# Optimization experiments

Hardware: AMD Instinct MI355X
Metric: run time of the kernel (lower is better)

## Reference

```python
import jax, jax.numpy as jnp
import numpy as np

D_MODEL = 2048
NQ = 16      # query heads
NKV = 4      # kv heads (GQA)
DH = 128     # content head dim
DR = 64      # rope head dim
DKV = 512    # kv latent dim
DQC = 1536   # q latent dim
B, S = 2, 2048
DT = DH + DR


def rotate_half(x):
    x1, x2 = jnp.split(x, 2, axis=-1)
    return jnp.concatenate([-x2, x1], axis=-1)


def setup_inputs() -> dict:
    key = jax.random.key(0)
    ks = jax.random.split(key, 10)
    sc = 0.02
    x = jax.random.normal(ks[0], (B, S, D_MODEL), jnp.float32)
    positions = jnp.arange(S, dtype=jnp.int32)
    # standard RoPE cache over the rope subspace
    inv_freq = 1.0 / (10000.0 ** (jnp.arange(0, DR, 2, dtype=jnp.float32) / DR))
    ang = positions.astype(jnp.float32)[:, None] * inv_freq[None, :]   # [S, DR/2]
    emb = jnp.concatenate([ang, ang], axis=-1)                         # [S, DR]
    cos_cache = jnp.cos(emb)
    sin_cache = jnp.sin(emb)
    attn_mask = jnp.tril(jnp.ones((S, S), dtype=bool))                 # causal, True=attend
    # weights stored [in, out] (torch Linear weight transposed)
    W_DKV = sc * jax.random.normal(ks[1], (D_MODEL, DKV), jnp.float32)
    W_UK = sc * jax.random.normal(ks[2], (DKV, NKV * DH), jnp.float32)
    W_UV = sc * jax.random.normal(ks[3], (DKV, NKV * DH), jnp.float32)
    W_DQ = sc * jax.random.normal(ks[4], (D_MODEL, DQC), jnp.float32)
    W_UQ = sc * jax.random.normal(ks[5], (DQC, NQ * DH), jnp.float32)
    W_KR = sc * jax.random.normal(ks[6], (D_MODEL, NKV * DR), jnp.float32)
    W_QR = sc * jax.random.normal(ks[7], (D_MODEL, NQ * DR), jnp.float32)
    W_O = sc * jax.random.normal(ks[8], (NQ * DH, D_MODEL), jnp.float32)
    return {"x": x, "cos_cache": cos_cache, "sin_cache": sin_cache,
            "positions": positions, "attn_mask": attn_mask,
            "W_DKV": W_DKV, "W_UK": W_UK, "W_UV": W_UV, "W_DQ": W_DQ,
            "W_UQ": W_UQ, "W_KR": W_KR, "W_QR": W_QR, "W_O": W_O}


def reference(x, cos_cache, sin_cache, positions, attn_mask,
              W_DKV, W_UK, W_UV, W_DQ, W_UQ, W_KR, W_QR, W_O):
    b, s, _ = x.shape
    cos = cos_cache[positions][None, None]  # [1,1,S,DR]
    sin = sin_cache[positions][None, None]
    # low-rank KV latent (this is the MLA cache)
    c_kv = x @ W_DKV                                                 # [B,S,DKV]
    K_rope = (x @ W_KR).reshape(b, s, NKV, DR).transpose(0, 2, 1, 3)  # [B,NKV,S,DR]
    K_rope = K_rope * cos + rotate_half(K_rope) * sin
    # decompress K/V content from latent
    K_content = (c_kv @ W_UK).reshape(b, s, NKV, DH).transpose(0, 2, 1, 3)  # [B,NKV,S,DH]
    V = (c_kv @ W_UV).reshape(b, s, NKV, DH).transpose(0, 2, 1, 3)          # [B,NKV,S,DH]
    # queries via low-rank path + rope subspace
    c_q = x @ W_DQ
    Q_content = (c_q @ W_UQ).reshape(b, s, NQ, DH).transpose(0, 2, 1, 3)    # [B,NQ,S,DH]
    Q_rope = (x @ W_QR).reshape(b, s, NQ, DR).transpose(0, 2, 1, 3)         # [B,NQ,S,DR]
    Q_rope = Q_rope * cos + rotate_half(Q_rope) * sin
    Q = jnp.concatenate([Q_content, Q_rope], axis=-1)   # [B,NQ,S,DT]
    K = jnp.concatenate([K_content, K_rope], axis=-1)   # [B,NKV,S,DT]
    # GQA: group query heads over shared kv heads (no materialized repeat)
    G = NQ // NKV
    Qg = Q.reshape(b, NKV, G, s, DT)
    scores = jnp.einsum('bkgsd,bktd->bkgst', Qg, K) / np.float32(np.sqrt(DT))
    scores = jnp.where(attn_mask[None, None, None], scores, -jnp.inf)
    w = jax.nn.softmax(scores, axis=-1)
    attn = jnp.einsum('bkgst,bktd->bkgsd', w, V)         # [B,NKV,G,S,DH]
    attn = attn.reshape(b, NQ, s, DH).transpose(0, 2, 1, 3).reshape(b, s, NQ * DH)
    out = attn @ W_O                                     # [B,S,D_MODEL]
    return out, c_kv, K_rope
```

## Files before the change

### kernel.cpp

```cpp
#include <hip/hip_runtime.h>
#include <stdint.h>

typedef unsigned short u16;
typedef unsigned int u32;

#define B_    2
#define S_    2048
#define NQ_   16
#define NKV_  4
#define DH_   128
#define DR_   64
#define DT_   192
#define M_    4096

using short8 = __attribute__((ext_vector_type(8))) short;
using f32x4  = __attribute__((ext_vector_type(4))) float;
using half8  = __attribute__((ext_vector_type(8))) _Float16;
using u16x4  = __attribute__((ext_vector_type(4))) u16;

__device__ __forceinline__ float cl(float f) {
    return fminf(fmaxf(f, -3.38e38f), 3.38e38f);
}
__device__ __forceinline__ u16 f2b(float f) {
    union { float f; u32 u; } v; v.f = f;
    u32 u = v.u;
    return (u16)((u + 0x7fffu + ((u >> 16) & 1u)) >> 16);
}
__device__ __forceinline__ void gload16(const void* g, void* l) {
    __builtin_amdgcn_global_load_lds(
        (const __attribute__((address_space(1))) void*)g,
        (__attribute__((address_space(3))) void*)l,
        16, 0, 0);
}

__device__ __forceinline__ void wt_body(const float* __restrict__ W,
                                        _Float16* __restrict__ T,
                                        int K, int N, int kx, int ny,
                                        float (*tile)[33]) {
    int k0 = kx * 32, n0 = ny * 32;
    int tx = threadIdx.x, ty = threadIdx.y;
#pragma unroll
    for (int i = 0; i < 32; i += 8)
        tile[ty + i][tx] = W[(size_t)(k0 + ty + i) * N + n0 + tx];
    __syncthreads();
#pragma unroll
    for (int i = 0; i < 32; i += 8)
        T[(size_t)(n0 + ty + i) * K + k0 + tx] = (_Float16)tile[tx][ty + i];
}

__global__ __launch_bounds__(256) void prep_all(const float* __restrict__ x,
                                                _Float16* __restrict__ xf,
                                                const float* __restrict__ W_DKV,
                                                const float* __restrict__ W_KR,
                                                const float* __restrict__ W_DQ,
                                                const float* __restrict__ W_QR,
                                                const float* __restrict__ W_UQ,
                                                const float* __restrict__ W_UK,
                                                const float* __restrict__ W_UV,
                                                const float* __restrict__ W_O,
                                                _Float16* __restrict__ Wmeg,
                                                _Float16* __restrict__ Wuq,
                                                _Float16* __restrict__ Wukv,
                                                _Float16* __restrict__ Wo) {
    __shared__ float tile[32][33];
    const int id = blockIdx.x;
    if (id < 1024) {
        wt_body(W_DKV, Wmeg, 2048, 512, id & 63, id >> 6, tile);
    } else if (id < 1536) {
        int l = id - 1024;
        wt_body(W_KR, Wmeg + (size_t)512 * 2048, 2048, 256, l & 63, l >> 6, tile);
    } else if (id < 4608) {
        int l = id - 1536;
        wt_body(W_DQ, Wmeg + (size_t)768 * 2048, 2048, 1536, l & 63, l >> 6, tile);
    } else if (id < 6656) {
        int l = id - 4608;
        wt_body(W_QR, Wmeg + (size_t)2304 * 2048, 2048, 1024, l & 63, l >> 6, tile);
    } else if (id < 9728) {
        int l = id - 6656;
        wt_body(W_UQ, Wuq, 1536, 2048, l % 48, l / 48, tile);
    } else if (id < 9984) {
        int l = id - 9728;
        wt_body(W_UK, Wukv, 512, 512, l & 15, l >> 4, tile);
    } else if (id < 10240) {
        int l = id - 9984;
        wt_body(W_UV, Wukv + (size_t)512 * 512, 512, 512, l & 15, l >> 4, tile);
    } else if (id < 14336) {
        int l = id - 10240;
        wt_body(W_O, Wo, 2048, 2048, l & 63, l >> 6, tile);
    } else {
        int l = id - 14336;
        int t1 = threadIdx.y * 32 + threadIdx.x;
        size_t i = ((size_t)l * 256 + t1) * 8;
        float4 a = *(const float4*)(x + i);
        float4 b4 = *(const float4*)(x + i + 4);
        float va[8] = {a.x, a.y, a.z, a.w, b4.x, b4.y, b4.z, b4.w};
        half8 f;
#pragma unroll
        for (int j = 0; j < 8; ++j) f[j] = (_Float16)va[j];
        *(half8*)(xf + i) = f;
    }
}

__device__ __forceinline__ void gemm_body(const _Float16* __restrict__ A, int lda,
                                          const _Float16* __restrict__ Bt,
                                          void* p0, void* p1, void* p2,
                                          void* p3, void* p4,
                                          float cscale, int mode,
                                          int N, int K, int bx,
                                          _Float16* lA, _Float16* lB) {
    const int t = threadIdx.x, lane = t & 63, w = t >> 6;
    const int quad = lane >> 4, l16 = lane & 15;
    const int wr = w >> 1, wc = w & 1;
    const int m0 = blockIdx.y * 128, n0 = bx * 128;
    f32x4 acc[4][4] = {};

    for (int kt = 0; kt < K; kt += 32) {
        __syncthreads();
#pragma unroll
        for (int c = 0; c < 2; ++c) {
            const int chunk = c * 256 + t;
            const int row = chunk >> 2, co = (chunk & 3) * 8;
            const int lofs = (c * 256 + w * 64) * 8;
            gload16(A + (size_t)(m0 + row) * lda + kt + co, lA + lofs);
            gload16(Bt + (size_t)(n0 + row) * K + kt + co, lB + lofs);
        }
        __syncthreads();
        half8 af[4], bf4[4];
#pragma unroll
        for (int i = 0; i < 4; ++i) {
            af[i]  = *(const half8*)&lA[(wr * 64 + i * 16 + l16) * 32 + quad * 8];
            bf4[i] = *(const half8*)&lB[(wc * 64 + i * 16 + l16) * 32 + quad * 8];
        }
#pragma unroll
        for (int i = 0; i < 4; ++i)
#pragma unroll
            for (int j = 0; j < 4; ++j)
                acc[i][j] = __builtin_amdgcn_mfma_f32_16x16x32_f16(af[i], bf4[j], acc[i][j], 0, 0, 0);
    }
#pragma unroll
    for (int i = 0; i < 4; ++i)
#pragma unroll
        for (int j = 0; j < 4; ++j) {
            const int mbase = m0 + wr * 64 + i * 16 + quad * 4;
            const int nn = n0 + wc * 64 + j * 16 + l16;
            if (mode == 0) {
                float* C = (float*)p0;
#pragma unroll
                for (int r = 0; r < 4; ++r)
                    C[(size_t)(mbase + r) * N + nn] = cl(acc[i][j][r]);
            } else if (mode == 2) {
                u16* Q = (u16*)p0;
                const int h = nn >> 7, dcol = nn & 127;
#pragma unroll
                for (int r = 0; r < 4; ++r)
                    Q[(size_t)(mbase + r) * 3072 + h * 192 + dcol] =
                        f2b(acc[i][j][r] * cscale);
            } else if (mode == 3) {
                const int bb = mbase >> 11, s = mbase & 2047;
                if (nn < 512) {
                    u16* Kp = (u16*)p0;
                    const int kv = nn >> 7, d = nn & 127;
                    const size_t rb = ((size_t)((bb * 4 + kv) * 2048 + s)) * 192 + d;
#pragma unroll
                    for (int r = 0; r < 4; ++r)
                        Kp[rb + (size_t)r * 192] = f2b(acc[i][j][r]);
                } else {
                    u16* Vt = (u16*)p1;
                    const int e = nn - 512, kv = e >> 7, d = e & 127;
                    u16x4 pk;
                    pk[0] = f2b(acc[i][j][0]); pk[1] = f2b(acc[i][j][1]);
                    pk[2] = f2b(acc[i][j][2]); pk[3] = f2b(acc[i][j][3]);
                    *(u16x4*)&((u16*)Vt)[((size_t)((bb * 4 + kv) * 128 + d)) * 2048 + s] = pk;
                }
            } else {
                if (nn < 512) {
                    float* ckv = (float*)p0;
                    _Float16* ckf = (_Float16*)p1;
#pragma unroll
                    for (int r = 0; r < 4; ++r) {
                        float v = acc[i][j][r];
                        ckv[(size_t)(mbase + r) * 512 + nn] = cl(v);
                        ckf[(size_t)(mbase + r) * 512 + nn] = (_Float16)v;
                    }
                } else if (nn < 768) {
                    float* krr = (float*)p2;
#pragma unroll
                    for (int r = 0; r < 4; ++r)
                        krr[(size_t)(mbase + r) * 256 + (nn - 512)] = acc[i][j][r];
                } else if (nn < 2304) {
                    _Float16* dqc = (_Float16*)p3;
#pragma unroll
                    for (int r = 0; r < 4; ++r)
                        dqc[(size_t)(mbase + r) * 1536 + (nn - 768)] = (_Float16)acc[i][j][r];
                } else {
                    _Float16* qrf = (_Float16*)p4;
#pragma unroll
                    for (int r = 0; r < 4; ++r)
                        qrf[(size_t)(mbase + r) * 1024 + (nn - 2304)] = (_Float16)acc[i][j][r];
                }
            }
        }
}

__global__ __launch_bounds__(256) void gemm_f16(const _Float16* __restrict__ A, int lda,
                                                const _Float16* __restrict__ Bt,
                                                void* p0, void* p1, void* p2,
                                                void* p3, void* p4,
                                                float cscale, int mode,
                                                int N, int K) {
    __shared__ __align__(16) _Float16 lA[128 * 32];
    __shared__ __align__(16) _Float16 lB[128 * 32];
    gemm_body(A, lda, Bt, p0, p1, p2, p3, p4, cscale, mode, N, K, blockIdx.x, lA, lB);
}

__global__ __launch_bounds__(256) void gemm_uqkv(const _Float16* __restrict__ dqc,
                                                 const _Float16* __restrict__ Wuq,
                                                 u16* __restrict__ qb16, float sc,
                                                 const _Float16* __restrict__ ckf,
                                                 const _Float16* __restrict__ Wukv,
                                                 u16* __restrict__ Kp,
                                                 u16* __restrict__ Vt) {
    __shared__ __align__(16) _Float16 lA[128 * 32];
    __shared__ __align__(16) _Float16 lB[128 * 32];
    const int bx = blockIdx.x;
    if (bx < 16)
        gemm_body(dqc, 1536, Wuq, qb16, nullptr, nullptr, nullptr, nullptr,
                  sc, 2, 2048, 1536, bx, lA, lB);
    else
        gemm_body(ckf, 512, Wukv, Kp, Vt, nullptr, nullptr, nullptr,
                  1.f, 3, 1024, 512, bx - 16, lA, lB);
}

__global__ __launch_bounds__(256) void rope_all(const _Float16* __restrict__ qrf,
                                                const float* __restrict__ krr,
                                                const float* __restrict__ cosc,
                                                const float* __restrict__ sinc,
                                                const int* __restrict__ pos,
                                                u16* __restrict__ qb16,
                                                float* __restrict__ Krope,
                                                u16* __restrict__ Kp) {
    const float sc = 0.07216878364870322f;
    if ((int)blockIdx.x < 8192) {
        int t = blockIdx.x * 256 + threadIdx.x;
        int d = t & 31, h = (t >> 5) & 15, rowi = t >> 9;
        int s = rowi & 2047;
        int p = pos[s];
        float c1 = cosc[p * 64 + d],      s1 = sinc[p * 64 + d];
        float c2 = cosc[p * 64 + 32 + d], s2 = sinc[p * 64 + 32 + d];
        const _Float16* base = qrf + (size_t)rowi * 1024 + h * 64;
        float x1 = (float)base[d];
        float x2 = (float)base[d + 32];
        u16* q = qb16 + (size_t)rowi * 3072 + h * 192 + 128;
        q[d]      = f2b((x1 * c1 - x2 * s1) * sc);
        q[d + 32] = f2b((x2 * c2 + x1 * s2) * sc);
    } else {
        int t = (blockIdx.x - 8192) * 256 + threadIdx.x;
        int d = t & 31, kv = (t >> 5) & 3, rowi = t >> 7;
        int b = rowi >> 11, s = rowi & 2047;
        int p = pos[s];
        float c1 = cosc[p * 64 + d],      s1 = sinc[p * 64 + d];
        float c2 = cosc[p * 64 + 32 + d], s2 = sinc[p * 64 + 32 + d];
        float x1 = krr[(size_t)rowi * 256 + kv * 64 + d];
        float x2 = krr[(size_t)rowi * 256 + kv * 64 + 32 + d];
        float o1 = x1 * c1 - x2 * s1;
        float o2 = x2 * c2 + x1 * s2;
        int g = b * NKV_ + kv;
        size_t ob = ((size_t)(g * S_) + s) * 64;
        Krope[ob + d]      = cl(o1);
        Krope[ob + 32 + d] = cl(o2);
        u16* kp = Kp + ((size_t)(g * S_ + s)) * 192 + 128;
        kp[d]      = f2b(o1);
        kp[32 + d] = f2b(o2);
    }
}

__global__ __launch_bounds__(256) void attn_mfma(const u16* __restrict__ qb16,
                                                 const u16* __restrict__ Kp,
                                                 const u16* __restrict__ Vt,
                                                 _Float16* __restrict__ atf) {
    __shared__ __align__(16) u16 lK[64 * 200];
    __shared__ __align__(16) u16 lVt[144 * 72];
    __shared__ __align__(16) u16 lP[4][16 * 72];

    const int t = threadIdx.x, lane = t & 63, w = t >> 6;
    const int quad = lane >> 4, l16 = lane & 15;
    const int id = blockIdx.x;
    const int g = id & 7;
    const int b = g >> 2;
    const int k = id >> 3;
    const int h = (g & 3) * 4 + (k & 3);
    const int px = k >> 2;

#pragma unroll
    for (int c = 0; c < 4; ++c) {
        int i = c * 256 + t;
        int rr = 128 + (i >> 6), ccol = i & 63;
        lVt[rr * 72 + ccol] = (rr == 128) ? (u16)0x3F80 : (u16)0;
    }

    for (int ph = 0; ph < 2; ++ph) {
        const int qt = ph ? px : (31 - px);
        const int q0 = qt * 64;
        const int iw = q0 + w * 16;

        short8 qf[6];
        {
            const u16* qp = qb16 + ((size_t)(b * S_ + iw + l16)) * 3072 + h * 192;
#pragma unroll
            for (int kc = 0; kc < 6; ++kc)
                qf[kc] = *(const short8*)&qp[kc * 32 + quad * 8];
        }

        f32x4 O9[9] = {};
        float mr[4] = {-1e30f, -1e30f, -1e30f, -1e30f};

        const int ntile = qt + 1;
        for (int tile = 0; tile < ntile; ++tile) {
            const int j0 = tile * 64;
            __syncthreads();
#pragma unroll
            for (int c = 0; c < 6; ++c) {
                int seg = c * 256 + t;
                int row = seg / 24, ch = (seg % 24) * 8;
                *(uint4*)&lK[row * 200 + ch] =
                    *(const uint4*)&Kp[((size_t)g * S_ + j0 + row) * 192 + ch];
            }
#pragma unroll
            for (int c = 0; c < 4; ++c) {
                int seg = c * 256 + t;
                int d = seg >> 3, ch = (seg & 7) * 8;
                *(uint4*)&lVt[d * 72 + ch] =
                    *(const uint4*)&Vt[((size_t)g * 128 + d) * S_ + j0 + ch];
            }
            __syncthreads();

            f32x4 s4[4];
            __builtin_amdgcn_s_setprio(1);
#pragma unroll
            for (int cc = 0; cc < 4; ++cc) {
                f32x4 sx = {};
#pragma unroll
                for (int kc = 0; kc < 6; ++kc) {
                    short8 kf = *(const short8*)&lK[(cc * 16 + l16) * 200 + kc * 32 + quad * 8];
                    sx = __builtin_amdgcn_mfma_f32_16x16x32_bf16(qf[kc], kf, sx, 0, 0, 0);
                }
                s4[cc] = sx;
            }
            __builtin_amdgcn_s_setprio(0);

            float sv[4][4];
#pragma unroll
            for (int cc = 0; cc < 4; ++cc)
#pragma unroll
                for (int r = 0; r < 4; ++r) {
                    int ir = iw + quad * 4 + r;
                    sv[cc][r] = (j0 + cc * 16 + l16 <= ir) ? s4[cc][r] : -1e30f;
                }
            float tm[4];
#pragma unroll
            for (int r = 0; r < 4; ++r)
                tm[r] = fmaxf(fmaxf(sv[0][r], sv[1][r]), fmaxf(sv[2][r], sv[3][r]));
#pragma unroll
            for (int m = 1; m < 16; m <<= 1)
#pragma unroll
                for (int r = 0; r < 4; ++r) tm[r] = fmaxf(tm[r], __shfl_xor(tm[r], m));
            int small = (tm[0] <= mr[0] + 8.f) && (tm[1] <= mr[1] + 8.f) &&
                        (tm[2] <= mr[2] + 8.f) && (tm[3] <= mr[3] + 8.f);
            if (!__all(small)) {
                float al[4];
#pragma unroll
                for (int r = 0; r < 4; ++r) {
                    float mn = fmaxf(mr[r], tm[r]);
                    al[r] = __expf(mr[r] - mn);
                    mr[r] = mn;
                }
#pragma unroll
                for (int dc = 0; dc < 9; ++dc)
#pragma unroll
                    for (int r = 0; r < 4; ++r) O9[dc][r] *= al[r];
            }
            float p[4][4];
#pragma unroll
            for (int cc = 0; cc < 4; ++cc)
#pragma unroll
                for (int r = 0; r < 4; ++r)
                    p[cc][r] = __expf(sv[cc][r] - mr[r]);
#pragma unroll
            for (int cc = 0; cc < 4; ++cc)
#pragma unroll
                for (int r = 0; r < 4; ++r)
                    lP[w][(quad * 4 + r) * 72 + cc * 16 + l16] = f2b(p[cc][r]);
            short8 pf0 = *(const short8*)&lP[w][l16 * 72 + quad * 8];
            short8 pf1 = *(const short8*)&lP[w][l16 * 72 + 32 + quad * 8];
            __builtin_amdgcn_s_setprio(1);
#pragma unroll
            for (int dc = 0; dc < 9; ++dc) {
                short8 vf0 = *(const short8*)&lVt[(dc * 16 + l16) * 72 + quad * 8];
                short8 vf1 = *(const short8*)&lVt[(dc * 16 + l16) * 72 + 32 + quad * 8];
                O9[dc] = __builtin_amdgcn_mfma_f32_16x16x32_bf16(pf0, vf0, O9[dc], 0, 0, 0);
                O9[dc] = __builtin_amdgcn_mfma_f32_16x16x32_bf16(pf1, vf1, O9[dc], 0, 0, 0);
            }
            __builtin_amdgcn_s_setprio(0);
        }
        float inv[4];
#pragma unroll
        for (int r = 0; r < 4; ++r) {
            float lr = __shfl(O9[8][r], quad * 16);
            inv[r] = 1.f / fmaxf(lr, 1e-30f);
        }
#pragma unroll
        for (int dc = 0; dc < 8; ++dc)
#pragma unroll
            for (int r = 0; r < 4; ++r) {
                int ir = iw + quad * 4 + r;
                atf[((size_t)(b * S_ + ir)) * 2048 + h * 128 + dc * 16 + l16] =
                    (_Float16)cl(O9[dc][r] * inv[r]);
            }
    }
}

extern "C" void kernel_launch(void* const* d_in, const int* in_sizes, int n_in,
                              void* d_out, int out_size, void* d_ws, size_t ws_size,
                              hipStream_t stream) {
    const float* x     = (const float*)d_in[0];
    const float* cosc  = (const float*)d_in[1];
    const float* sinc  = (const float*)d_in[2];
    const int*   pos   = (const int*)d_in[3];
    const float* W_DKV = (const float*)d_in[5];
    const float* W_UK  = (const float*)d_in[6];
    const float* W_UV  = (const float*)d_in[7];
    const float* W_DQ  = (const float*)d_in[8];
    const float* W_UQ  = (const float*)d_in[9];
    const float* W_KR  = (const float*)d_in[10];
    const float* W_QR  = (const float*)d_in[11];
    const float* W_O   = (const float*)d_in[12];
    (void)ws_size;

    float* outp      = (float*)d_out;
    float* ckv_out   = outp + 8388608;
    float* krope_out = outp + 10485760;

    char* w = (char*)d_ws;
    auto alloc = [&](size_t bytes) { char* p = w; w += bytes; return p; };
    _Float16* xf   = (_Float16*)alloc(16777216);
    _Float16* ckf  = (_Float16*)alloc(4194304);
    float*    krr  = (float*)alloc(4194304);
    _Float16* dqc  = (_Float16*)alloc(12582912);
    _Float16* qrf  = (_Float16*)alloc(8388608);
    u16*      qb16 = (u16*)alloc(25165824);
    u16*      Kp   = (u16*)alloc(6291456);
    u16*      Vt   = (u16*)alloc(4194304);
    _Float16* atf  = (_Float16*)alloc(16777216);
    _Float16* Wmeg = (_Float16*)alloc(13631488);
    _Float16* Wuq  = (_Float16*)alloc(6291456);
    _Float16* Wukv = (_Float16*)alloc(1048576);
    _Float16* Wo   = (_Float16*)alloc(8388608);

    const float sc = 0.07216878364870322f;

    prep_all<<<18432, dim3(32, 8), 0, stream>>>(x, xf,
                                                W_DKV, W_KR, W_DQ, W_QR,
                                                W_UQ, W_UK, W_UV, W_O,
                                                Wmeg, Wuq, Wukv, Wo);

    gemm_f16<<<dim3(26, 32), 256, 0, stream>>>(xf, 2048, Wmeg,
                                               ckv_out, ckf, krr, dqc, qrf,
                                               1.f, 6, 3328, 2048);
    gemm_uqkv<<<dim3(24, 32), 256, 0, stream>>>(dqc, Wuq, qb16, sc,
                                                ckf, Wukv, Kp, Vt);

    rope_all<<<10240, 256, 0, stream>>>(qrf, krr, cosc, sinc, pos,
                                        qb16, krope_out, Kp);

    attn_mfma<<<512, 256, 0, stream>>>(qb16, Kp, Vt, atf);
    gemm_f16<<<dim3(16, 32), 256, 0, stream>>>(atf, 2048, Wo,
                                               outp, nullptr, nullptr, nullptr, nullptr,
                                               1.f, 0, 2048, 2048);
}
```

Baseline: 484.1 us.

## Add 256x256 swizzled-LDS GEMM kernel for large projections

Adds a new 512-thread GEMM kernel with 256x256 output tiles, a K-step of 64, XOR-swizzled LDS layout and a grouped block-index remap for L2 locality. It is used for the fused down-projection, the Q up-projection and the output projection. The small KV up-projection stays on the old 128x128 kernel, which now runs as a separate launch instead of being merged with the Q up-projection. Larger tiles raise data reuse per block and cut LDS bank conflicts, but they launch fewer blocks (128–208), which may leave many of the 256 CUs idle, and they raise register and LDS pressure.

Result: no change. 482.5 us (-0.3%).

```diff
diff --git a/kernel.cpp b/kernel.cpp
--- a/kernel.cpp
+++ b/kernel.cpp
@@ -103,8 +103,7 @@
 
 __device__ __forceinline__ void gemm_body(const _Float16* __restrict__ A, int lda,
                                           const _Float16* __restrict__ Bt,
-                                          void* p0, void* p1, void* p2,
-                                          void* p3, void* p4,
+                                          void* p0, void* p1,
                                           float cscale, int mode,
                                           int N, int K, int bx,
                                           _Float16* lA, _Float16* lB) {
@@ -143,19 +142,7 @@
         for (int j = 0; j < 4; ++j) {
             const int mbase = m0 + wr * 64 + i * 16 + quad * 4;
             const int nn = n0 + wc * 64 + j * 16 + l16;
-            if (mode == 0) {
-                float* C = (float*)p0;
-#pragma unroll
-                for (int r = 0; r < 4; ++r)
-                    C[(size_t)(mbase + r) * N + nn] = cl(acc[i][j][r]);
-            } else if (mode == 2) {
-                u16* Q = (u16*)p0;
-                const int h = nn >> 7, dcol = nn & 127;
-#pragma unroll
-                for (int r = 0; r < 4; ++r)
-                    Q[(size_t)(mbase + r) * 3072 + h * 192 + dcol] =
-                        f2b(acc[i][j][r] * cscale);
-            } else if (mode == 3) {
+            if (mode == 3) {
                 const int bb = mbase >> 11, s = mbase & 2047;
                 if (nn < 512) {
                     u16* Kp = (u16*)p0;
@@ -173,6 +160,93 @@
                     *(u16x4*)&((u16*)Vt)[((size_t)((bb * 4 + kv) * 128 + d)) * 2048 + s] = pk;
                 }
             } else {
+                float* C = (float*)p0;
+#pragma unroll
+                for (int r = 0; r < 4; ++r)
+                    C[(size_t)(mbase + r) * N + nn] = cl(acc[i][j][r]);
+            }
+        }
+}
+
+__global__ __launch_bounds__(256) void gemm_f16(const _Float16* __restrict__ A, int lda,
+                                                const _Float16* __restrict__ Bt,
+                                                void* p0, void* p1,
+                                                float cscale, int mode,
+                                                int N, int K) {
+    __shared__ __align__(16) _Float16 lA[128 * 32];
+    __shared__ __align__(16) _Float16 lB[128 * 32];
+    gemm_body(A, lda, Bt, p0, p1, cscale, mode, N, K, blockIdx.x, lA, lB);
+}
+
+__global__ __launch_bounds__(512) void gemm256(const _Float16* __restrict__ A, int lda,
+                                               const _Float16* __restrict__ Bt,
+                                               void* p0, void* p1, void* p2,
+                                               void* p3, void* p4,
+                                               float cscale, int mode,
+                                               int N, int K, int NBX) {
+    __shared__ __align__(16) _Float16 lA[256 * 64];
+    __shared__ __align__(16) _Float16 lB[256 * 64];
+    const int t = threadIdx.x, lane = t & 63, w = t >> 6;
+    const int quad = lane >> 4, l16 = lane & 15;
+    const int wr = w >> 2, wc = w & 3;
+    const int id = blockIdx.x;
+    const int cpx = (NBX * 16) >> 3;
+    const int swz = (id & 7) * cpx + (id >> 3);
+    const int bx = swz % NBX, by = swz / NBX;
+    const int m0 = by * 256, n0 = bx * 256;
+    f32x4 acc[8][4] = {};
+
+    for (int kt = 0; kt < K; kt += 64) {
+        __syncthreads();
+#pragma unroll
+        for (int q = 0; q < 4; ++q) {
+            const int chunk = q * 512 + t;
+            const int row = chunk >> 3, cop = chunk & 7;
+            const int co = (cop ^ (row & 7)) * 8;
+            const int lofs = (q * 512 + w * 64) * 8;
+            gload16(A + (size_t)(m0 + row) * lda + kt + co, lA + lofs);
+            gload16(Bt + (size_t)(n0 + row) * K + kt + co, lB + lofs);
+        }
+        __syncthreads();
+#pragma unroll
+        for (int kc = 0; kc < 2; ++kc) {
+            half8 af[8], bf[4];
+#pragma unroll
+            for (int i = 0; i < 8; ++i) {
+                const int r = wr * 128 + i * 16 + l16;
+                af[i] = *(const half8*)&lA[(r * 8 + ((kc * 4 + quad) ^ (r & 7))) * 8];
+            }
+#pragma unroll
+            for (int j = 0; j < 4; ++j) {
+                const int r = wc * 64 + j * 16 + l16;
+                bf[j] = *(const half8*)&lB[(r * 8 + ((kc * 4 + quad) ^ (r & 7))) * 8];
+            }
+#pragma unroll
+            for (int i = 0; i < 8; ++i)
+#pragma unroll
+                for (int j = 0; j < 4; ++j)
+                    acc[i][j] = __builtin_amdgcn_mfma_f32_16x16x32_f16(af[i], bf[j], acc[i][j], 0, 0, 0);
+        }
+    }
+#pragma unroll
+    for (int i = 0; i < 8; ++i)
+#pragma unroll
+        for (int j = 0; j < 4; ++j) {
+            const int mbase = m0 + wr * 128 + i * 16 + quad * 4;
+            const int nn = n0 + wc * 64 + j * 16 + l16;
+            if (mode == 0) {
+                float* C = (float*)p0;
+#pragma unroll
+                for (int r = 0; r < 4; ++r)
+                    C[(size_t)(mbase + r) * N + nn] = cl(acc[i][j][r]);
+            } else if (mode == 2) {
+                u16* Q = (u16*)p0;
+                const int h = nn >> 7, dcol = nn & 127;
+#pragma unroll
+                for (int r = 0; r < 4; ++r)
+                    Q[(size_t)(mbase + r) * 3072 + h * 192 + dcol] =
+                        f2b(acc[i][j][r] * cscale);
+            } else {
                 if (nn < 512) {
                     float* ckv = (float*)p0;
                     _Float16* ckf = (_Float16*)p1;
@@ -200,35 +274,6 @@
                 }
             }
         }
-}
-
-__global__ __launch_bounds__(256) void gemm_f16(const _Float16* __restrict__ A, int lda,
-                                                const _Float16* __restrict__ Bt,
-                                                void* p0, void* p1, void* p2,
-                                                void* p3, void* p4,
-                                                float cscale, int mode,
-                                                int N, int K) {
-    __shared__ __align__(16) _Float16 lA[128 * 32];
-    __shared__ __align__(16) _Float16 lB[128 * 32];
-    gemm_body(A, lda, Bt, p0, p1, p2, p3, p4, cscale, mode, N, K, blockIdx.x, lA, lB);
-}
-
-__global__ __launch_bounds__(256) void gemm_uqkv(const _Float16* __restrict__ dqc,
-                                                 const _Float16* __restrict__ Wuq,
-                                                 u16* __restrict__ qb16, float sc,
-                                                 const _Float16* __restrict__ ckf,
-                                                 const _Float16* __restrict__ Wukv,
-                                                 u16* __restrict__ Kp,
-                                                 u16* __restrict__ Vt) {
-    __shared__ __align__(16) _Float16 lA[128 * 32];
-    __shared__ __align__(16) _Float16 lB[128 * 32];
-    const int bx = blockIdx.x;
-    if (bx < 16)
-        gemm_body(dqc, 1536, Wuq, qb16, nullptr, nullptr, nullptr, nullptr,
-                  sc, 2, 2048, 1536, bx, lA, lB);
-    else
-        gemm_body(ckf, 512, Wukv, Kp, Vt, nullptr, nullptr, nullptr,
-                  1.f, 3, 1024, 512, bx - 16, lA, lB);
 }
 
 __global__ __launch_bounds__(256) void rope_all(const _Float16* __restrict__ qrf,
@@ -463,17 +508,20 @@
                                                 W_UQ, W_UK, W_UV, W_O,
                                                 Wmeg, Wuq, Wukv, Wo);
 
-    gemm_f16<<<dim3(26, 32), 256, 0, stream>>>(xf, 2048, Wmeg,
-                                               ckv_out, ckf, krr, dqc, qrf,
-                                               1.f, 6, 3328, 2048);
-    gemm_uqkv<<<dim3(24, 32), 256, 0, stream>>>(dqc, Wuq, qb16, sc,
-                                                ckf, Wukv, Kp, Vt);
+    gemm256<<<208, 512, 0, stream>>>(xf, 2048, Wmeg,
+                                     ckv_out, ckf, krr, dqc, qrf,
+                                     1.f, 6, 3328, 2048, 13);
+    gemm256<<<128, 512, 0, stream>>>(dqc, 1536, Wuq,
+                                     qb16, nullptr, nullptr, nullptr, nullptr,
+                                     sc, 2, 2048, 1536, 8);
+    gemm_f16<<<dim3(8, 32), 256, 0, stream>>>(ckf, 512, Wukv,
+                                              Kp, Vt, 1.f, 3, 1024, 512);
 
     rope_all<<<10240, 256, 0, stream>>>(qrf, krr, cosc, sinc, pos,
                                         qb16, krope_out, Kp);
 
     attn_mfma<<<512, 256, 0, stream>>>(qb16, Kp, Vt, atf);
-    gemm_f16<<<dim3(16, 32), 256, 0, stream>>>(atf, 2048, Wo,
-                                               outp, nullptr, nullptr, nullptr, nullptr,
-                                               1.f, 0, 2048, 2048);
-}
+    gemm256<<<128, 512, 0, stream>>>(atf, 2048, Wo,
+                                     outp, nullptr, nullptr, nullptr, nullptr,
+                                     1.f, 0, 2048, 2048, 8);
+}
```
